# Optimization experiments

Hardware: AMD Instinct MI355X
Metric: run time of the kernel (lower is better)

Reference implementation:

```python
import jax, jax.numpy as jnp
import numpy as np

B, T, D_IN = 1024, 128, 256
H = 128          # hidden_dim == memory_unit_size (required by einsum)
M = 128          # memory_units == memory_unit_size (required by view)
W = 128          # memory_unit_size
R = 4            # read_heads
OUT = 2


def setup_inputs() -> dict:
    key = jax.random.key(0)
    ks = jax.random.split(key, 9)
    s = 0.05
    return {
        "x": jax.random.normal(ks[0], (B, T, D_IN), dtype=jnp.float32),
        "memory": jax.random.normal(ks[1], (M, W), dtype=jnp.float32) * s,
        "read_vectors0": jax.random.normal(ks[2], (R, W), dtype=jnp.float32) * s,
        "W_ih": jax.random.normal(ks[3], (4 * H, D_IN + R * W), dtype=jnp.float32) * s,
        "W_hh": jax.random.normal(ks[4], (4 * H, H), dtype=jnp.float32) * s,
        "b_ih": jax.random.normal(ks[5], (4 * H,), dtype=jnp.float32) * s,
        "b_hh": jax.random.normal(ks[6], (4 * H,), dtype=jnp.float32) * s,
        "fc_w": jax.random.normal(ks[7], (OUT, H + R * W), dtype=jnp.float32) * s,
        "fc_b": jax.random.normal(ks[8], (OUT,), dtype=jnp.float32) * s,
    }


def reference(x, memory, read_vectors0, W_ih, W_hh, b_ih, b_hh, fc_w, fc_b):
    batch = x.shape[0]
    # softmax over memory slots (dim=0), constant across timesteps
    mem_sm = jax.nn.softmax(memory, axis=0)  # [M, W]
    bias = b_ih + b_hh

    # initial read vectors: [R, W] -> repeat over batch -> flatten [B, R*W]
    rv = jnp.tile(read_vectors0[None], (batch, 1, 1)).reshape(batch, R * W)
    h0 = jnp.zeros((batch, H), x.dtype)
    c0 = jnp.zeros((batch, H), x.dtype)

    def step(carry, xt):
        h, c, rv = carry
        inp = jnp.concatenate([xt, rv], axis=-1)           # [B, D_IN+R*W]
        gates = inp @ W_ih.T + h @ W_hh.T + bias           # [B, 4H]
        i, f, g, o = jnp.split(gates, 4, axis=-1)          # torch LSTM gate order
        c = jax.nn.sigmoid(f) * c + jax.nn.sigmoid(i) * jnp.tanh(g)
        h = jax.nn.sigmoid(o) * jnp.tanh(c)                # [B, H]
        read = jnp.einsum('ij,kj->ki', mem_sm, h)          # [B, M]
        # faithful to torch: repeat to [R, B, M] then view(B, R*M) (mixes rows)
        rv_new = jnp.broadcast_to(read[None], (R, batch, M)).reshape(batch, R * M)
        out = jnp.concatenate([h, rv_new], axis=-1) @ fc_w.T + fc_b  # [B, OUT]
        return (h, c, rv_new), out

    _, outs = jax.lax.scan(step, (h0, c0, rv), jnp.swapaxes(x, 0, 1))  # [T, B, OUT]
    return outs.mean(axis=0)  # [B, OUT]
```

## Files before the change

kernel.cpp:

```cpp
#include <hip/hip_runtime.h>

#define BB 1024
#define TT 128
#define NBLK 256

using bf16   = __bf16;
using bf16x8 = __attribute__((ext_vector_type(8))) bf16;
using bf16x4 = __attribute__((ext_vector_type(4))) bf16;
using f32x4  = __attribute__((ext_vector_type(4))) float;

__device__ __forceinline__ float fsig(float x) {
  return __builtin_amdgcn_rcpf(1.f + __expf(-x));
}
__device__ __forceinline__ float ftanh(float x) {
  return 2.f * __builtin_amdgcn_rcpf(1.f + __expf(-2.f * x)) - 1.f;
}

__device__ __forceinline__ void st_i32_coh(int* p, int v) {
  __hip_atomic_store(p, v, __ATOMIC_RELAXED, __HIP_MEMORY_SCOPE_AGENT);
}
__device__ __forceinline__ int ld_i32_coh(const int* p) {
  return __hip_atomic_load((int*)p, __ATOMIC_RELAXED, __HIP_MEMORY_SCOPE_AGENT);
}
__device__ __forceinline__ float ld_f32_coh(const float* p) {
  return __hip_atomic_load((float*)p, __ATOMIC_RELAXED, __HIP_MEMORY_SCOPE_AGENT);
}
__device__ __forceinline__ void st_f32_coh(float* p, float v) {
  __hip_atomic_store(p, v, __ATOMIC_RELAXED, __HIP_MEMORY_SCOPE_AGENT);
}
__device__ __forceinline__ void st_u16_coh(unsigned short* p, unsigned short v) {
  __hip_atomic_store(p, v, __ATOMIC_RELAXED, __HIP_MEMORY_SCOPE_AGENT);
}
__device__ __forceinline__ bf16x8 ld_bf16x8_coh(const bf16* p) {
  union { unsigned long long u[2]; bf16x8 v; } c;
  c.u[0] = __hip_atomic_load((unsigned long long*)p, __ATOMIC_RELAXED, __HIP_MEMORY_SCOPE_AGENT);
  c.u[1] = __hip_atomic_load((unsigned long long*)(p + 4), __ATOMIC_RELAXED, __HIP_MEMORY_SCOPE_AGENT);
  return c.v;
}

__global__ void x_convert(const float* __restrict__ x, bf16* __restrict__ x_bf,
                          int* __restrict__ slots) {
  const int tid = threadIdx.x, bid = blockIdx.x;
  if (bid == 0) {
    for (int e = tid; e < 4096; e += 256) st_i32_coh(slots + e, 0);
  }
  const int lane = tid & 63, wv = tid >> 6;
  const int wg = bid * 4 + wv;
#pragma unroll 4
  for (int r = 0; r < 16; ++r) {
    int rid = wg + r * 8192;
    int b = rid >> 7, t = rid & 127;
    int rowp = ((b >> 4) & 15) * 64 + (b >> 8) * 16 + (b & 15);
    const float4 v = *(const float4*)(x + (size_t)rid * 256 + lane * 4);
    bf16x4 o;
    o[0] = (bf16)v.x; o[1] = (bf16)v.y; o[2] = (bf16)v.z; o[3] = (bf16)v.w;
    *(bf16x4*)(x_bf + ((size_t)t * BB + rowp) * 256 + lane * 4) = o;
  }
}

__global__ void __launch_bounds__(256, 1) dnc_main(
    const bf16* __restrict__ x_bf, const float* __restrict__ memf,
    const float* __restrict__ rv0,
    const float* __restrict__ W_ih, const float* __restrict__ W_hh,
    const float* __restrict__ b_ih, const float* __restrict__ b_hh,
    const float* __restrict__ fc_w, const float* __restrict__ fc_b,
    bf16* __restrict__ hbuf0, bf16* __restrict__ hbuf1,
    float* __restrict__ hsumG, int* __restrict__ slots,
    float* __restrict__ out) {
  __shared__ bf16 sWx[32][264];
  __shared__ bf16 sWhh[32][136];
  __shared__ bf16 sWM[32][520];
  __shared__ bf16 sHq[16][520];
  __shared__ bf16 smT[128][136];
  __shared__ float sFM[2][512];
  __shared__ float sG0[32];

  const int bid = blockIdx.x, tid = threadIdx.x;
  const int rt = bid >> 4, gt = bid & 15;
  const int wave = tid >> 6, lane = tid & 63;
  const int l15 = lane & 15, l4 = lane >> 4;

  auto gcol = [&](int pos) { return ((pos >> 3) << 7) + gt * 8 + (pos & 7); };

  for (int e = tid; e < 32 * 256; e += 256) sWx[e >> 8][e & 255] = (bf16)W_ih[(size_t)gcol(e >> 8) * 768 + (e & 255)];
  for (int e = tid; e < 32 * 128; e += 256) sWhh[e >> 7][e & 127] = (bf16)W_hh[gcol(e >> 7) * 128 + (e & 127)];
  if (tid < 128) {
    const int n = tid;
    float mx = -1e30f;
    for (int m = 0; m < 128; ++m) mx = fmaxf(mx, memf[m * 128 + n]);
    float s = 0.f;
    for (int m = 0; m < 128; ++m) s += __expf(memf[m * 128 + n] - mx);
    float inv = __builtin_amdgcn_rcpf(s);
    float fa[8] = {0.f, 0.f, 0.f, 0.f, 0.f, 0.f, 0.f, 0.f};
#pragma unroll 4
    for (int m = 0; m < 128; ++m) {
      float e = __expf(memf[m * 128 + n] - mx) * inv;
      smT[n][m] = (bf16)e;
#pragma unroll
      for (int o = 0; o < 2; ++o)
#pragma unroll
        for (int r = 0; r < 4; ++r) fa[o * 4 + r] += e * fc_w[o * 640 + 128 + r * 128 + m];
    }
#pragma unroll
    for (int o = 0; o < 2; ++o)
#pragma unroll
      for (int r = 0; r < 4; ++r) sFM[o][r * 128 + n] = fa[o * 4 + r];
  }
  if (tid < 32) {
    const int c = tid >> 3, jj = tid & 7;
    const float* wr = W_ih + (size_t)(c * 128 + gt * 8 + jj) * 768 + 256;
    float acc = 0.f;
#pragma unroll 4
    for (int k4 = 0; k4 < 128; ++k4) {
      float4 a = *(const float4*)(rv0 + k4 * 4);
      float4 b = *(const float4*)(wr + k4 * 4);
      acc += a.x * b.x + a.y * b.y + a.z * b.z + a.w * b.w;
    }
    sG0[tid] = acc;
  }
  __syncthreads();
#pragma unroll
  for (int r = 0; r < 4; ++r) {
    bf16x8 afr[2][4];
#pragma unroll
    for (int g = 0; g < 2; ++g)
#pragma unroll
      for (int kk = 0; kk < 4; ++kk) {
        const float* ap = W_ih + (size_t)gcol(g * 16 + l15) * 768 + 256 + r * 128 + kk * 32 + l4 * 8;
        float4 p0 = *(const float4*)ap, p1 = *(const float4*)(ap + 4);
        bf16x8 f;
        f[0] = (bf16)p0.x; f[1] = (bf16)p0.y; f[2] = (bf16)p0.z; f[3] = (bf16)p0.w;
        f[4] = (bf16)p1.x; f[5] = (bf16)p1.y; f[6] = (bf16)p1.z; f[7] = (bf16)p1.w;
        afr[g][kk] = f;
      }
#pragma unroll
    for (int nto = 0; nto < 2; ++nto) {
      const int nt = wave * 2 + nto;
      f32x4 a0 = {0.f, 0.f, 0.f, 0.f}, a1 = {0.f, 0.f, 0.f, 0.f};
#pragma unroll
      for (int kk = 0; kk < 4; ++kk) {
        bf16x8 b = *(const bf16x8*)&smT[nt * 16 + l15][kk * 32 + l4 * 8];
        a0 = __builtin_amdgcn_mfma_f32_16x16x32_bf16(afr[0][kk], b, a0, 0, 0, 0);
        a1 = __builtin_amdgcn_mfma_f32_16x16x32_bf16(afr[1][kk], b, a1, 0, 0, 0);
      }
#pragma unroll
      for (int reg = 0; reg < 4; ++reg) {
        sWM[l4 * 4 + reg][r * 128 + nt * 16 + l15]      = (bf16)a0[reg];
        sWM[16 + l4 * 4 + reg][r * 128 + nt * 16 + l15] = (bf16)a1[reg];
      }
    }
  }
  __syncthreads();

  const float bv0 = b_ih[gcol(l15)] + b_hh[gcol(l15)];
  const float bv1 = b_ih[gcol(16 + l15)] + b_hh[gcol(16 + l15)];

  const bool lo = (l15 < 8);
  const int j = l15 & 7;
  const int rb = lo ? 0 : 2;
  float cst[2] = {0.f, 0.f}, hsum[2] = {0.f, 0.f};
  int growp[2];
#pragma unroll
  for (int k = 0; k < 2; ++k) growp[k] = rt * 16 + (l4 * 4 + rb + k) + 256 * wave;

  f32x4 acc0, acc1;

  auto xpart = [&](int t) {
    acc0 = f32x4{bv0, bv0, bv0, bv0};
    acc1 = f32x4{bv1, bv1, bv1, bv1};
    const bf16* xr = x_bf + ((size_t)t * BB + rt * 64 + wave * 16 + l15) * 256 + l4 * 8;
#pragma unroll
    for (int kk = 0; kk < 8; ++kk) {
      bf16x8 a  = *(const bf16x8*)(xr + kk * 32);
      bf16x8 w0 = *(const bf16x8*)&sWx[l15][kk * 32 + l4 * 8];
      bf16x8 w1 = *(const bf16x8*)&sWx[16 + l15][kk * 32 + l4 * 8];
      acc0 = __builtin_amdgcn_mfma_f32_16x16x32_bf16(a, w0, acc0, 0, 0, 0);
      acc1 = __builtin_amdgcn_mfma_f32_16x16x32_bf16(a, w1, acc1, 0, 0, 0);
    }
  };

  auto hpart = [&](const bf16* hrd) {
    bf16x8 ha[4];
    const bf16* hr = hrd + (size_t)(rt * 16 + l15 + 256 * wave) * 128 + l4 * 8;
#pragma unroll
    for (int kk = 0; kk < 4; ++kk) ha[kk] = ld_bf16x8_coh(hr + kk * 32);
#pragma unroll
    for (int pass = 0; pass < 4; ++pass) {
      int row = (tid >> 4) + 16 * pass, seg = tid & 15;
      bf16x8 v = ld_bf16x8_coh(hrd + (size_t)(rt * 64 + row) * 128 + seg * 8);
      *(bf16x8*)&sHq[row >> 2][(row & 3) * 128 + seg * 8] = v;
    }
#pragma unroll
    for (int kk = 0; kk < 4; ++kk) {
      bf16x8 w0 = *(const bf16x8*)&sWhh[l15][kk * 32 + l4 * 8];
      bf16x8 w1 = *(const bf16x8*)&sWhh[16 + l15][kk * 32 + l4 * 8];
      acc0 = __builtin_amdgcn_mfma_f32_16x16x32_bf16(ha[kk], w0, acc0, 0, 0, 0);
      acc1 = __builtin_amdgcn_mfma_f32_16x16x32_bf16(ha[kk], w1, acc1, 0, 0, 0);
    }
    __syncthreads();
#pragma unroll
    for (int kk = 0; kk < 16; ++kk) {
      bf16x8 a  = *(const bf16x8*)&sHq[l15][kk * 32 + l4 * 8];
      bf16x8 w0 = *(const bf16x8*)&sWM[l15][kk * 32 + l4 * 8];
      bf16x8 w1 = *(const bf16x8*)&sWM[16 + l15][kk * 32 + l4 * 8];
      acc0 = __builtin_amdgcn_mfma_f32_16x16x32_bf16(a, w0, acc0, 0, 0, 0);
      acc1 = __builtin_amdgcn_mfma_f32_16x16x32_bf16(a, w1, acc1, 0, 0, 0);
    }
  };

  auto pw = [&](bool add_g0, bf16* hwr) {
    float o0[4], o1[4];
#pragma unroll
    for (int r = 0; r < 4; ++r) {
      o0[r] = __shfl_xor(acc0[r], 8);
      o1[r] = __shfl_xor(acc1[r], 8);
    }
    float g0i = 0.f, g0f = 0.f, g0g = 0.f, g0o = 0.f;
    if (add_g0) {
      g0i = sG0[j]; g0f = sG0[8 + j]; g0g = sG0[16 + j]; g0o = sG0[24 + j];
    }
#pragma unroll
    for (int k = 0; k < 2; ++k) {
      int r = rb + k;
      float gi = (lo ? acc0[r] : o0[r]) + g0i;
      float gf = (lo ? o0[r] : acc0[r]) + g0f;
      float gg = (lo ? acc1[r] : o1[r]) + g0g;
      float go = (lo ? o1[r] : acc1[r]) + g0o;
      cst[k] = fsig(gf) * cst[k] + fsig(gi) * ftanh(gg);
      float h = fsig(go) * ftanh(cst[k]);
      hsum[k] += h;
      union { bf16 b; unsigned short u; } cv; cv.b = (bf16)h;
      st_u16_coh((unsigned short*)(hwr + (size_t)growp[k] * 128 + gt * 8 + j), cv.u);
    }
  };

  auto commit = [&](int gen) {
    asm volatile("s_waitcnt vmcnt(0)" ::: "memory");
    __syncthreads();
    if (tid == 0) st_i32_coh(slots + bid * 16, gen);
  };
  auto gridwait = [&](int gen) {
    if (wave == 0) {
      int s0, s1, s2, s3;
      do {
        s0 = ld_i32_coh(slots + lane * 16);
        s1 = ld_i32_coh(slots + (lane + 64) * 16);
        s2 = ld_i32_coh(slots + (lane + 128) * 16);
        s3 = ld_i32_coh(slots + (lane + 192) * 16);
      } while (min(min(s0, s1), min(s2, s3)) < gen);
    }
    __syncthreads();
  };

  xpart(0);
  pw(true, hbuf0);
  commit(1);
  for (int t = 1; t < TT; ++t) {
    xpart(t);
    gridwait(t);
    hpart((t & 1) ? hbuf0 : hbuf1);
    pw(false, (t & 1) ? hbuf1 : hbuf0);
    commit(t + 1);
  }
#pragma unroll
  for (int k = 0; k < 2; ++k)
    st_f32_coh(hsumG + (size_t)growp[k] * 128 + gt * 8 + j, hsum[k]);
  commit(TT + 1);
  gridwait(TT + 1);
  {
    int row = bid * 4 + wave;
    const float* hsr = hsumG + (size_t)row * 128;
    const float* hqr = hsumG + (size_t)(row & 255) * 512;
    float s0 = 0.f, s1 = 0.f;
    for (int k = lane; k < 128; k += 64) { float v = ld_f32_coh(hsr + k); s0 += v * fc_w[k]; s1 += v * fc_w[640 + k]; }
    for (int k = lane; k < 512; k += 64) { float v = ld_f32_coh(hqr + k); s0 += v * sFM[0][k]; s1 += v * sFM[1][k]; }
    for (int off = 32; off > 0; off >>= 1) { s0 += __shfl_down(s0, off); s1 += __shfl_down(s1, off); }
    if (lane == 0) {
      out[row * 2 + 0] = s0 * (1.f / 128.f) + fc_b[0];
      out[row * 2 + 1] = s1 * (1.f / 128.f) + fc_b[1];
    }
  }
}

extern "C" void kernel_launch(void* const* d_in, const int* in_sizes, int n_in,
                              void* d_out, int out_size, void* d_ws, size_t ws_size,
                              hipStream_t stream) {
  const float* x      = (const float*)d_in[0];
  const float* memory = (const float*)d_in[1];
  const float* rv0    = (const float*)d_in[2];
  const float* W_ih   = (const float*)d_in[3];
  const float* W_hh   = (const float*)d_in[4];
  const float* b_ih   = (const float*)d_in[5];
  const float* b_hh   = (const float*)d_in[6];
  const float* fc_w   = (const float*)d_in[7];
  const float* fc_b   = (const float*)d_in[8];
  float* out = (float*)d_out;
  char* ws = (char*)d_ws;

  bf16* x_bf   = (bf16*)ws;
  bf16* hbuf0  = (bf16*)(ws + 67108864);
  bf16* hbuf1  = (bf16*)(ws + 67371008);
  int*  slots  = (int*)(ws + 67633152);
  float* hsumG = (float*)(ws + 67649536);

  x_convert<<<2048, 256, 0, stream>>>(x, x_bf, slots);
  dnc_main<<<NBLK, 256, 0, stream>>>(x_bf, memory, rv0, W_ih, W_hh, b_ih, b_hh,
                                     fc_w, fc_b, hbuf0, hbuf1, hsumG, slots, out);
}
```

Before: 925.3 us.

## Replace global grid barrier with dependency-only waits and coalesce h stores

After: 929.0 us. No clear change (+0.4%).

```diff
diff --git a/kernel.cpp b/kernel.cpp
--- a/kernel.cpp
+++ b/kernel.cpp
@@ -28,7 +28,7 @@
 __device__ __forceinline__ void st_f32_coh(float* p, float v) {
   __hip_atomic_store(p, v, __ATOMIC_RELAXED, __HIP_MEMORY_SCOPE_AGENT);
 }
-__device__ __forceinline__ void st_u16_coh(unsigned short* p, unsigned short v) {
+__device__ __forceinline__ void st_u64_coh(unsigned long long* p, unsigned long long v) {
   __hip_atomic_store(p, v, __ATOMIC_RELAXED, __HIP_MEMORY_SCOPE_AGENT);
 }
 __device__ __forceinline__ bf16x8 ld_bf16x8_coh(const bf16* p) {
@@ -74,6 +74,7 @@
   __shared__ bf16 smT[128][136];
   __shared__ float sFM[2][512];
   __shared__ float sG0[32];
+  __shared__ bf16 sHoutT[8][72];
 
   const int bid = blockIdx.x, tid = threadIdx.x;
   const int rt = bid >> 4, gt = bid & 15;
@@ -81,6 +82,16 @@
   const int l15 = lane & 15, l4 = lane >> 4;
 
   auto gcol = [&](int pos) { return ((pos >> 3) << 7) + gt * 8 + (pos & 7); };
+
+  int myDep = 0;
+  {
+    const int idx = tid >> 4;
+    int rg = rt;
+    if (idx >= 1 && idx <= 4) rg = 4 * (rt & 3) + (idx - 1);
+    else if (idx >= 5 && idx <= 8) rg = (rt >> 2) + 4 * (idx - 5);
+    myDep = rg * 16 + (tid & 15);
+  }
+  const bool amPoller = (tid < 144);
 
   for (int e = tid; e < 32 * 256; e += 256) sWx[e >> 8][e & 255] = (bf16)W_ih[(size_t)gcol(e >> 8) * 768 + (e & 255)];
   for (int e = tid; e < 32 * 128; e += 256) sWhh[e >> 7][e & 127] = (bf16)W_hh[gcol(e >> 7) * 128 + (e & 127)];
@@ -158,6 +169,7 @@
   const bool lo = (l15 < 8);
   const int j = l15 & 7;
   const int rb = lo ? 0 : 2;
+  const int lrow = wave * 16 + l4 * 4 + rb;
   float cst[2] = {0.f, 0.f}, hsum[2] = {0.f, 0.f};
   int growp[2];
 #pragma unroll
@@ -208,7 +220,7 @@
     }
   };
 
-  auto pw = [&](bool add_g0, bf16* hwr) {
+  auto pw = [&](bool add_g0) {
     float o0[4], o1[4];
 #pragma unroll
     for (int r = 0; r < 4; ++r) {
@@ -219,6 +231,7 @@
     if (add_g0) {
       g0i = sG0[j]; g0f = sG0[8 + j]; g0g = sG0[16 + j]; g0o = sG0[24 + j];
     }
+    float hv[2];
 #pragma unroll
     for (int k = 0; k < 2; ++k) {
       int r = rb + k;
@@ -227,46 +240,55 @@
       float gg = (lo ? acc1[r] : o1[r]) + g0g;
       float go = (lo ? o1[r] : acc1[r]) + g0o;
       cst[k] = fsig(gf) * cst[k] + fsig(gi) * ftanh(gg);
-      float h = fsig(go) * ftanh(cst[k]);
-      hsum[k] += h;
-      union { bf16 b; unsigned short u; } cv; cv.b = (bf16)h;
-      st_u16_coh((unsigned short*)(hwr + (size_t)growp[k] * 128 + gt * 8 + j), cv.u);
-    }
-  };
-
-  auto commit = [&](int gen) {
+      hv[k] = fsig(go) * ftanh(cst[k]);
+      hsum[k] += hv[k];
+    }
+    union { bf16 h[2]; unsigned u; } pk;
+    pk.h[0] = (bf16)hv[0]; pk.h[1] = (bf16)hv[1];
+    *(unsigned*)&sHoutT[j][lrow] = pk.u;
+  };
+
+  auto commit = [&](int gen, bf16* hwr) {
+    __syncthreads();
+    if (tid < 64) {
+      const int w = tid >> 4, rr = tid & 15;
+      const int grow = rt * 16 + rr + 256 * w;
+      union { bf16 h[8]; unsigned long long u[2]; } pk;
+#pragma unroll
+      for (int q = 0; q < 8; ++q) pk.h[q] = sHoutT[q][tid];
+      unsigned long long* dst = (unsigned long long*)(hwr + (size_t)grow * 128 + gt * 8);
+      st_u64_coh(dst, pk.u[0]);
+      st_u64_coh(dst + 1, pk.u[1]);
+    }
     asm volatile("s_waitcnt vmcnt(0)" ::: "memory");
     __syncthreads();
     if (tid == 0) st_i32_coh(slots + bid * 16, gen);
   };
   auto gridwait = [&](int gen) {
-    if (wave == 0) {
-      int s0, s1, s2, s3;
-      do {
-        s0 = ld_i32_coh(slots + lane * 16);
-        s1 = ld_i32_coh(slots + (lane + 64) * 16);
-        s2 = ld_i32_coh(slots + (lane + 128) * 16);
-        s3 = ld_i32_coh(slots + (lane + 192) * 16);
-      } while (min(min(s0, s1), min(s2, s3)) < gen);
+    if (amPoller) {
+      while (ld_i32_coh(slots + myDep * 16) < gen) {}
     }
     __syncthreads();
   };
 
   xpart(0);
-  pw(true, hbuf0);
-  commit(1);
+  pw(true);
+  commit(1, hbuf0);
   for (int t = 1; t < TT; ++t) {
     xpart(t);
     gridwait(t);
     hpart((t & 1) ? hbuf0 : hbuf1);
-    pw(false, (t & 1) ? hbuf1 : hbuf0);
-    commit(t + 1);
+    pw(false);
+    commit(t + 1, (t & 1) ? hbuf1 : hbuf0);
   }
 #pragma unroll
   for (int k = 0; k < 2; ++k)
     st_f32_coh(hsumG + (size_t)growp[k] * 128 + gt * 8 + j, hsum[k]);
-  commit(TT + 1);
-  gridwait(TT + 1);
+  asm volatile("s_waitcnt vmcnt(0)" ::: "memory");
+  __syncthreads();
+  if (tid == 0) st_i32_coh(slots + bid * 16, TT + 2);
+  while (ld_i32_coh(slots + tid * 16) < TT + 2) {}
+  __syncthreads();
   {
     int row = bid * 4 + wave;
     const float* hsr = hsumG + (size_t)row * 128;
```
